# Kernel tuning notes

Hardware: AMD Instinct MI355X
Metric: run time of the kernel (lower is better)

Reference implementation:

```python
import jax, jax.numpy as jnp
import numpy as np

N, D = 131072, 512
G, NG = 512, 256  # G groups of equal size NG, contiguous; N == G*NG
MARGIN, LAMBDA_CD, LAMBDA_CDD, LAMBDA_PCC, K_MARGIN = 2.0, 0.0, 1.0, 1.0, 0.02
EPS = 1e-6


def setup_inputs() -> dict:
    key = jax.random.key(0)
    k1, k2, k3, k4 = jax.random.split(key, 4)
    z_r = jax.random.normal(k1, (N, D), jnp.float32)
    z_r = z_r / jnp.linalg.norm(z_r, axis=-1, keepdims=True)
    z_v = jax.random.normal(k2, (N, D), jnp.float32)
    z_v = z_v / jnp.linalg.norm(z_v, axis=-1, keepdims=True)
    labels = jax.random.randint(k3, (N,), 0, 2)
    groups = jnp.repeat(jnp.arange(G), NG)  # contiguous equal-size groups
    var_lens = jax.random.randint(k4, (N,), 0, 10000)
    return {"z_r": z_r, "z_v": z_v, "labels": labels, "groups": groups, "var_lens": var_lens}


def reference(z_r, z_v, labels, groups, var_lens):
    # cosine distance per pair: [N]
    d = 1.0 - jnp.sum(z_r * z_v, axis=-1)

    mb = (labels == 0).astype(d.dtype)
    mp = (labels == 1).astype(d.dtype)
    nb, npos = mb.sum(), mp.sum()
    db_mean = jnp.sum(d * mb) / jnp.maximum(nb, 1.0)
    dp_mean = jnp.sum(d * mp) / jnp.maximum(npos, 1.0)

    l_cd = jnp.where(nb > 0, db_mean, 0.0)
    l_cdd = jnp.where((nb > 0) & (npos > 0),
                      jax.nn.relu(MARGIN + db_mean - dp_mean), 0.0)

    # --- per-group losses, vectorized over G equal-size contiguous groups ---
    d_g = d.reshape(G, NG)                                   # [G, n_g]
    v_g = var_lens.reshape(G, NG).astype(d.dtype)            # [G, n_g]

    # Pearson-style z-score matching loss (torch std is unbiased, ddof=1)
    v_std = jnp.std(v_g, axis=1, ddof=1)
    d_std = jnp.std(d_g, axis=1, ddof=1)
    v_z = (v_g - v_g.mean(axis=1, keepdims=True)) / (v_std + EPS)[:, None]
    d_z = (d_g - d_g.mean(axis=1, keepdims=True)) / (d_std + EPS)[:, None]
    corr_loss = jnp.mean((v_z - d_z) ** 2, axis=1)
    corr_loss = jnp.where((v_std > 0) & (d_std > 0), corr_loss, 0.0)

    # sort each group by var_len
    order = jnp.argsort(v_g, axis=1)
    v_s = jnp.take_along_axis(v_g, order, axis=1)            # [G, n_g]
    d_s = jnp.take_along_axis(d_g, order, axis=1)            # [G, n_g]

    # neighbor monotonicity violation
    neigh_viol = jnp.mean(jax.nn.relu(d_s[:, :-1] - d_s[:, 1:] + K_MARGIN), axis=1)

    # pairwise rank loss: dv[g,i,j] = v_s[g,j] - v_s[g,i] (matches torch unsqueeze(0)-unsqueeze(1))
    dv = v_s[:, None, :] - v_s[:, :, None]                   # [G, n_g, n_g]
    dd = d_s[:, None, :] - d_s[:, :, None]                   # [G, n_g, n_g]
    mask = (dv > 0).astype(d.dtype)
    cnt = mask.sum(axis=(1, 2))
    pair_sum = jnp.sum(jax.nn.relu(K_MARGIN - dd) * mask, axis=(1, 2))
    rank_loss = jnp.where(cnt > 0, pair_sum / jnp.maximum(cnt, 1.0), 0.0)

    group_loss = corr_loss + neigh_viol + rank_loss          # [G]
    # size-weighted sum; all groups have equal size NG -> plain mean
    l_pcc = jnp.mean(group_loss)

    total = LAMBDA_CD * l_cd + LAMBDA_CDD * l_cdd + LAMBDA_PCC * l_pcc
    return total, l_cdd, l_pcc, d
```

## Files before the change

kernel.cpp:

```cpp
#include <hip/hip_runtime.h>

#define NTOT   131072
#define GCNT   512
#define NGRP   256
#define KMARG  0.02f
#define CMARG  2.0f
#define EPSC   1e-6f

typedef float f4 __attribute__((ext_vector_type(4)));

template <int CTRL>
__device__ __forceinline__ float dpp_add(float v) {
  const int t = __builtin_amdgcn_update_dpp(0, __float_as_int(v), CTRL, 0xF, 0xF, true);
  return v + __int_as_float(t);
}
__device__ __forceinline__ float row16_sum(float v) {
  v = dpp_add<0x111>(v);
  v = dpp_add<0x112>(v);
  v = dpp_add<0x114>(v);
  v = dpp_add<0x118>(v);
  return v;
}

template <int NW, int M>
__device__ __forceinline__ void block_sum_m(float* v, float* red) {
  const int t = threadIdx.x;
#pragma unroll
  for (int m = 0; m < M; ++m) {
#pragma unroll
    for (int off = 32; off; off >>= 1) v[m] += __shfl_down(v[m], off, 64);
  }
  __syncthreads();
  if ((t & 63) == 0) {
#pragma unroll
    for (int m = 0; m < M; ++m) red[(t >> 6) * M + m] = v[m];
  }
  __syncthreads();
#pragma unroll
  for (int m = 0; m < M; ++m) {
    float s = 0.0f;
#pragma unroll
    for (int i = 0; i < NW; ++i) s += red[i * M + m];
    v[m] = s;
  }
}

__global__ __launch_bounds__(256, 2) void fused_kernel(const float* __restrict__ zr,
                                                       const float* __restrict__ zv,
                                                       const int* __restrict__ labels,
                                                       const int* __restrict__ varl,
                                                       float* __restrict__ dvec,
                                                       float* __restrict__ gout) {
  __shared__ float  red[4 * 4];
  __shared__ float  sd[NGRP];
  __shared__ float2 skv[NGRP];
  __shared__ float  sdat[NGRP];
  const int g = blockIdx.x, t = threadIdx.x;
  const int wave = t >> 6, lane = t & 63;
  const int l16 = lane & 15, sub = lane >> 4;
  const size_t rowbase = (size_t)g * NGRP;

#pragma unroll 1
  for (int it = 0; it < 16; ++it) {
    const int rg = it * 16 + wave * 4 + sub;
    const f4* ra = (const f4*)zr + ((rowbase + (size_t)rg) << 7);
    const f4* rb = (const f4*)zv + ((rowbase + (size_t)rg) << 7);
    f4 A[8], B[8];
#pragma unroll
    for (int k = 0; k < 8; ++k) A[k] = ra[l16 + 16 * k];
#pragma unroll
    for (int k = 0; k < 8; ++k) {
      const int kk = (k + 4) & 7;
      B[kk] = rb[l16 + 16 * kk];
    }
    f4 e = A[0] * B[0] + A[2] * B[2];
    f4 o = A[1] * B[1] + A[3] * B[3];
    e += A[4] * B[4];
    o += A[5] * B[5];
    e += A[6] * B[6];
    o += A[7] * B[7];
    const f4 s4 = e + o;
    float s = (s4.x + s4.y) + (s4.z + s4.w);
    s = row16_sum(s);
    if (l16 == 15) {
      const float dval = 1.0f - s;
      sd[rg] = dval;
      __builtin_nontemporal_store(dval, dvec + rowbase + rg);
    }
  }
  __syncthreads();

  const int idx = g * NGRP + t;
  const float dv  = sd[t];
  const float vv  = (float)varl[idx];
  const int   lab = labels[idx];

  skv[t] = make_float2(vv, dv);

  float sA[4] = {dv, vv, (lab == 0) ? dv : 0.0f, (lab == 0) ? 1.0f : 0.0f};
  block_sum_m<4, 4>(sA, red);
  const float sumd = sA[0], sumv = sA[1], sb = sA[2], cb = sA[3];
  const float md = sumd * (1.0f / NGRP), mv = sumv * (1.0f / NGRP);

  const float vdev = vv - mv, ddev = dv - md;
  float sB[3] = {vdev * vdev, ddev * ddev, vdev * ddev};
  block_sum_m<4, 3>(sB, red);
  const float svv = sB[0], sdd = sB[1], svd = sB[2];
  const float vstd = sqrtf(svv * (1.0f / (NGRP - 1)));
  const float dstd = sqrtf(sdd * (1.0f / (NGRP - 1)));
  const float iv = 1.0f / (vstd + EPSC), id = 1.0f / (dstd + EPSC);
  float corr = (svv * iv * iv + sdd * id * id - 2.0f * svd * iv * id) * (1.0f / NGRP);
  corr = (vstd > 0.0f && dstd > 0.0f) ? corr : 0.0f;

  int rank = 0;
  float pc = 0.0f, ps = 0.0f;
  const float pre = KMARG + dv;
  for (int j = 0; j < NGRP; ++j) {
    const float2 kv = skv[j];
    const float vj = kv.x, dj = kv.y;
    if (vj > vv) {
      pc += 1.0f;
      ps += fmaxf(pre - dj, 0.0f);
    }
    rank += (vj < vv || (vj == vv && j < t)) ? 1 : 0;
  }
  sdat[rank] = dv;
  __syncthreads();
  const float nv = (t < NGRP - 1) ? fmaxf(sdat[t] - sdat[t + 1] + KMARG, 0.0f) : 0.0f;

  float sC[3] = {ps, pc, nv};
  block_sum_m<4, 3>(sC, red);
  const float rank_loss = (sC[1] > 0.0f) ? sC[0] / fmaxf(sC[1], 1.0f) : 0.0f;
  const float neigh = sC[2] * (1.0f / (NGRP - 1));

  if (t == 0) {
    gout[g]            = corr + neigh + rank_loss;
    gout[GCNT + g]     = sb;
    gout[2 * GCNT + g] = cb;
    gout[3 * GCNT + g] = sumd;
  }
}

__global__ __launch_bounds__(512) void final_kernel(const float* __restrict__ gout,
                                                    float* __restrict__ out) {
  __shared__ float red[8 * 4];
  const int t = threadIdx.x;
  float s[4] = {gout[t], gout[GCNT + t], gout[2 * GCNT + t], gout[3 * GCNT + t]};
  block_sum_m<8, 4>(s, red);
  if (t == 0) {
    const float L = s[0], SB = s[1], CB = s[2], SumD = s[3];
    const float SP = SumD - SB;
    const float CP = (float)NTOT - CB;
    const float db = SB / fmaxf(CB, 1.0f);
    const float dp = SP / fmaxf(CP, 1.0f);
    const float l_cdd = (CB > 0.0f && CP > 0.0f) ? fmaxf(CMARG + db - dp, 0.0f) : 0.0f;
    const float l_pcc = L * (1.0f / GCNT);
    out[0] = l_cdd + l_pcc;
    out[1] = l_cdd;
    out[2] = l_pcc;
  }
}

extern "C" void kernel_launch(void* const* d_in, const int* in_sizes, int n_in,
                              void* d_out, int out_size, void* d_ws, size_t ws_size,
                              hipStream_t stream) {
  const float* zr     = (const float*)d_in[0];
  const float* zv     = (const float*)d_in[1];
  const int*   labels = (const int*)d_in[2];
  const int*   varl   = (const int*)d_in[4];
  float* out  = (float*)d_out;
  float* dvec = out + 3;
  float* gws  = (float*)d_ws;

  fused_kernel<<<GCNT, 256, 0, stream>>>(zr, zv, labels, varl, dvec, gws);
  final_kernel<<<1, 512, 0, stream>>>(gws, out);
}
```

Measured before the change: 130.8 us.

## Use 1024-thread blocks for the dot-product phase and batch the d-vector store

Grows each group's block from 256 to 1024 threads, so every wave handles 16 rows in 4 iterations instead of 16 rows spread over 16 iterations across 4 waves. This exposes more memory-level parallelism for the streaming z_r/z_v loads. The per-row d values are now written to global memory with one coalesced store after the sync instead of scattered single-lane stores. A scheduling barrier forces all loads to issue before the FMAs. The rank and statistics phase still uses only 256 threads, so three quarters of the block sit idle there, and the larger block may limit how many blocks stay resident per CU.

```diff
diff --git a/kernel.cpp b/kernel.cpp
--- a/kernel.cpp
+++ b/kernel.cpp
@@ -3,6 +3,8 @@
 #define NTOT   131072
 #define GCNT   512
 #define NGRP   256
+#define BS     1024
+#define NWAVE  (BS / 64)
 #define KMARG  0.02f
 #define CMARG  2.0f
 #define EPSC   1e-6f
@@ -45,13 +47,13 @@
   }
 }
 
-__global__ __launch_bounds__(256, 2) void fused_kernel(const float* __restrict__ zr,
-                                                       const float* __restrict__ zv,
-                                                       const int* __restrict__ labels,
-                                                       const int* __restrict__ varl,
-                                                       float* __restrict__ dvec,
-                                                       float* __restrict__ gout) {
-  __shared__ float  red[4 * 4];
+__global__ __launch_bounds__(BS, 4) void fused_kernel(const float* __restrict__ zr,
+                                                      const float* __restrict__ zv,
+                                                      const int* __restrict__ labels,
+                                                      const int* __restrict__ varl,
+                                                      float* __restrict__ dvec,
+                                                      float* __restrict__ gout) {
+  __shared__ float  red[NWAVE * 4];
   __shared__ float  sd[NGRP];
   __shared__ float2 skv[NGRP];
   __shared__ float  sdat[NGRP];
@@ -61,20 +63,18 @@
   const size_t rowbase = (size_t)g * NGRP;
 
 #pragma unroll 1
-  for (int it = 0; it < 16; ++it) {
-    const int rg = it * 16 + wave * 4 + sub;
+  for (int it = 0; it < 4; ++it) {
+    const int rg = wave * 16 + it * 4 + sub;
     const f4* ra = (const f4*)zr + ((rowbase + (size_t)rg) << 7);
     const f4* rb = (const f4*)zv + ((rowbase + (size_t)rg) << 7);
     f4 A[8], B[8];
 #pragma unroll
     for (int k = 0; k < 8; ++k) A[k] = ra[l16 + 16 * k];
 #pragma unroll
-    for (int k = 0; k < 8; ++k) {
-      const int kk = (k + 4) & 7;
-      B[kk] = rb[l16 + 16 * kk];
-    }
-    f4 e = A[0] * B[0] + A[2] * B[2];
-    f4 o = A[1] * B[1] + A[3] * B[3];
+    for (int k = 0; k < 8; ++k) B[k] = rb[l16 + 16 * k];
+    __builtin_amdgcn_sched_barrier(0);
+    f4 e = A[0] * B[0] + A[1] * B[1];
+    f4 o = A[2] * B[2] + A[3] * B[3];
     e += A[4] * B[4];
     o += A[5] * B[5];
     e += A[6] * B[6];
@@ -82,29 +82,30 @@
     const f4 s4 = e + o;
     float s = (s4.x + s4.y) + (s4.z + s4.w);
     s = row16_sum(s);
-    if (l16 == 15) {
-      const float dval = 1.0f - s;
-      sd[rg] = dval;
-      __builtin_nontemporal_store(dval, dvec + rowbase + rg);
-    }
+    if (l16 == 15) sd[rg] = 1.0f - s;
   }
   __syncthreads();
+  if (t < NGRP) __builtin_nontemporal_store(sd[t], dvec + rowbase + t);
 
-  const int idx = g * NGRP + t;
-  const float dv  = sd[t];
-  const float vv  = (float)varl[idx];
-  const int   lab = labels[idx];
-
-  skv[t] = make_float2(vv, dv);
+  const bool act = (t < NGRP);
+  float dv = 0.0f, vv = 0.0f;
+  int lab = -1;
+  if (act) {
+    dv = sd[t];
+    vv = (float)varl[rowbase + t];
+    lab = labels[rowbase + t];
+    skv[t] = make_float2(vv, dv);
+  }
 
   float sA[4] = {dv, vv, (lab == 0) ? dv : 0.0f, (lab == 0) ? 1.0f : 0.0f};
-  block_sum_m<4, 4>(sA, red);
+  block_sum_m<NWAVE, 4>(sA, red);
   const float sumd = sA[0], sumv = sA[1], sb = sA[2], cb = sA[3];
   const float md = sumd * (1.0f / NGRP), mv = sumv * (1.0f / NGRP);
 
-  const float vdev = vv - mv, ddev = dv - md;
+  const float vdev = act ? (vv - mv) : 0.0f;
+  const float ddev = act ? (dv - md) : 0.0f;
   float sB[3] = {vdev * vdev, ddev * ddev, vdev * ddev};
-  block_sum_m<4, 3>(sB, red);
+  block_sum_m<NWAVE, 3>(sB, red);
   const float svv = sB[0], sdd = sB[1], svd = sB[2];
   const float vstd = sqrtf(svv * (1.0f / (NGRP - 1)));
   const float dstd = sqrtf(sdd * (1.0f / (NGRP - 1)));
@@ -112,24 +113,26 @@
   float corr = (svv * iv * iv + sdd * id * id - 2.0f * svd * iv * id) * (1.0f / NGRP);
   corr = (vstd > 0.0f && dstd > 0.0f) ? corr : 0.0f;
 
+  float pc = 0.0f, ps = 0.0f;
   int rank = 0;
-  float pc = 0.0f, ps = 0.0f;
-  const float pre = KMARG + dv;
-  for (int j = 0; j < NGRP; ++j) {
-    const float2 kv = skv[j];
-    const float vj = kv.x, dj = kv.y;
-    if (vj > vv) {
-      pc += 1.0f;
-      ps += fmaxf(pre - dj, 0.0f);
+  if (act) {
+    const float pre = KMARG + dv;
+    for (int j = 0; j < NGRP; ++j) {
+      const float2 kv = skv[j];
+      const float vj = kv.x, dj = kv.y;
+      if (vj > vv) {
+        pc += 1.0f;
+        ps += fmaxf(pre - dj, 0.0f);
+      }
+      rank += (vj < vv || (vj == vv && j < t)) ? 1 : 0;
     }
-    rank += (vj < vv || (vj == vv && j < t)) ? 1 : 0;
+    sdat[rank] = dv;
   }
-  sdat[rank] = dv;
   __syncthreads();
   const float nv = (t < NGRP - 1) ? fmaxf(sdat[t] - sdat[t + 1] + KMARG, 0.0f) : 0.0f;
 
   float sC[3] = {ps, pc, nv};
-  block_sum_m<4, 3>(sC, red);
+  block_sum_m<NWAVE, 3>(sC, red);
   const float rank_loss = (sC[1] > 0.0f) ? sC[0] / fmaxf(sC[1], 1.0f) : 0.0f;
   const float neigh = sC[2] * (1.0f / (NGRP - 1));
 
@@ -172,6 +175,6 @@
   float* dvec = out + 3;
   float* gws  = (float*)d_ws;
 
-  fused_kernel<<<GCNT, 256, 0, stream>>>(zr, zv, labels, varl, dvec, gws);
+  fused_kernel<<<GCNT, BS, 0, stream>>>(zr, zv, labels, varl, dvec, gws);
   final_kernel<<<1, 512, 0, stream>>>(gws, out);
 }
```

New measurement: 160.7 us. +22.9%, slower.
